# Kernel optimization log

Hardware: AMD Instinct MI355X
Metric: run time of the kernel (lower is better)

Reference implementation:

```python
import jax, jax.numpy as jnp
import numpy as np
import math

V, E, N, L, S_BLOCK, R = 50257, 1024, 16, 8, 1024, 4
B, S = 2, 1024
H = E // N
IPAD = 0


def layer_norm(x, w, b, eps=1e-5):
    mu = jnp.mean(x, axis=-1, keepdims=True)
    var = jnp.mean(jnp.square(x - mu), axis=-1, keepdims=True)
    return (x - mu) * jax.lax.rsqrt(var + eps) * w + b


def setup_inputs():
    key = jax.random.key(0)
    ks = jax.random.split(key, 10)
    nrm = lambda k, shape: jax.random.normal(k, shape, jnp.float32) * 0.02
    return {
        "x": jax.random.randint(ks[0], (B, S), 1, V, dtype=jnp.int32),
        "tok_emb": nrm(ks[1], (V, E)),
        "pos_emb": nrm(ks[2], (S_BLOCK, E)),
        "dec_ln_w": jnp.ones((E,), jnp.float32),
        "dec_ln_b": jnp.zeros((E,), jnp.float32),
        "qkv_w": nrm(ks[3], (L, 3 * E, E)),
        "qkv_b": jnp.zeros((L, 3 * E), jnp.float32),
        "attn_proj_w": nrm(ks[4], (L, E, E)),
        "attn_proj_b": jnp.zeros((L, E), jnp.float32),
        "ln1_w": jnp.ones((L, E), jnp.float32),
        "ln1_b": jnp.zeros((L, E), jnp.float32),
        "fc_w": nrm(ks[5], (L, R * E, E)),
        "fc_b": jnp.zeros((L, R * E), jnp.float32),
        "mlp_proj_w": nrm(ks[6], (L, E, R * E)),
        "mlp_proj_b": jnp.zeros((L, E), jnp.float32),
        "ln2_w": jnp.ones((L, E), jnp.float32),
        "ln2_b": jnp.zeros((L, E), jnp.float32),
        "fin_ln_w": jnp.ones((E,), jnp.float32),
        "fin_ln_b": jnp.zeros((E,), jnp.float32),
    }


def _forward(x, tok_emb, pos_emb, dec_ln_w, dec_ln_b, qkv_w, qkv_b,
             attn_proj_w, attn_proj_b, ln1_w, ln1_b, fc_w, fc_b,
             mlp_proj_w, mlp_proj_b, ln2_w, ln2_b, fin_ln_w, fin_ln_b):
    # token + positional embedding
    h = tok_emb[x] + pos_emb[:S][None, :, :]  # [B,S,E]
    # attention mask: causal AND key-not-pad (ipad=0, no cache -> C=0)
    causal = jnp.tril(jnp.ones((S, S), bool))  # [S,S]
    keypad = (x != IPAD)  # [B,S]
    mask = causal[None, None, :, :] & keypad[:, None, None, :]  # [B,1,S,S]
    scale = 1.0 / math.sqrt(H)

    # Decoder: ln then dropout(eval no-op) before blocks
    h = layer_norm(h, dec_ln_w, dec_ln_b)

    def block(h, p):
        (qw, qb, pw, pb, l1w, l1b, fw, fb, mw, mb, l2w, l2b) = p
        qkv = h @ qw.T + qb  # [B,S,3E]
        q, k, v = jnp.split(qkv, 3, axis=-1)
        q = q.reshape(B, S, N, H).transpose(0, 2, 1, 3)  # [B,N,S,H]
        k = k.reshape(B, S, N, H).transpose(0, 2, 1, 3)
        v = v.reshape(B, S, N, H).transpose(0, 2, 1, 3)
        scores = jnp.einsum('bnsh,bnth->bnst', q, k) * scale  # [B,N,S,S]
        scores = jnp.where(mask, scores, -jnp.inf)
        attn = jax.nn.softmax(scores, axis=-1)
        o = jnp.einsum('bnst,bnth->bnsh', attn, v)
        o = o.transpose(0, 2, 1, 3).reshape(B, S, E)
        o = o @ pw.T + pb
        h = layer_norm(o + h, l1w, l1b)  # post-norm
        m = jax.nn.gelu(h @ fw.T + fb, approximate=False) @ mw.T + mb
        h = layer_norm(m + h, l2w, l2b)
        return h, None

    params = (qkv_w, qkv_b, attn_proj_w, attn_proj_b, ln1_w, ln1_b,
              fc_w, fc_b, mlp_proj_w, mlp_proj_b, ln2_w, ln2_b)
    h, _ = jax.lax.scan(block, h, params)
    # final Transformer LayerNorm
    return layer_norm(h, fin_ln_w, fin_ln_b)


def reference(x, tok_emb, pos_emb, dec_ln_w, dec_ln_b, qkv_w, qkv_b,
              attn_proj_w, attn_proj_b, ln1_w, ln1_b, fc_w, fc_b,
              mlp_proj_w, mlp_proj_b, ln2_w, ln2_b, fin_ln_w, fin_ln_b):
    return _forward(x, tok_emb, pos_emb, dec_ln_w, dec_ln_b, qkv_w, qkv_b,
                    attn_proj_w, attn_proj_b, ln1_w, ln1_b, fc_w, fc_b,
                    mlp_proj_w, mlp_proj_b, ln2_w, ln2_b, fin_ln_w, fin_ln_b)
```

## Files before the change

### kernel.cpp

```cpp
#include <hip/hip_runtime.h>
#include <hip/hip_bf16.h>

#define E 1024
#define SLEN 1024
#define QKV3 3072
#define HD 64

typedef unsigned short u16;
typedef unsigned int   u32;
typedef __bf16 bf16x8 __attribute__((ext_vector_type(8)));
typedef float  f32x4  __attribute__((ext_vector_type(4)));
typedef float  fv4    __attribute__((ext_vector_type(4)));
typedef u32    uv2    __attribute__((ext_vector_type(2)));

__device__ __forceinline__ u16 f2bf(float f) {
  __hip_bfloat16 h = __float2bfloat16(f);
  return __builtin_bit_cast(u16, h);
}
__device__ __forceinline__ u32 pk2(float a, float b) {
  return (u32)f2bf(a) | ((u32)f2bf(b) << 16);
}
__device__ __forceinline__ uint4 pack8(const float4& x, const float4& y) {
  return make_uint4(pk2(x.x,x.y), pk2(x.z,x.w), pk2(y.x,y.y), pk2(y.z,y.w));
}

__device__ __forceinline__ void gload16(const u16* g, u16* l) {
  __builtin_amdgcn_global_load_lds(
      (const __attribute__((address_space(1))) void*)g,
      (__attribute__((address_space(3))) void*)l, 16, 0, 0);
}

__device__ __forceinline__ int swzP(int row, int ch) { return (row<<4) + (ch ^ (row & 7)); }

__global__ __launch_bounds__(256)
void f2b(const float* __restrict__ src, u16* __restrict__ dst, int n4)
{
  const int stride = gridDim.x * 256;
  const fv4* s4 = (const fv4*)src;
  uv2* d2 = (uv2*)dst;
  for (int i = blockIdx.x * 256 + threadIdx.x; i < n4; i += stride) {
    const fv4 v = __builtin_nontemporal_load(s4 + i);
    uv2 o; o.x = pk2(v.x, v.y); o.y = pk2(v.z, v.w);
    d2[i] = o;
  }
}

template<int BN, int OUTBF, int GELU, int SK>
__global__ __launch_bounds__(256)
void gemm_lds(const u16* __restrict__ A, const u16* __restrict__ W,
              const float* __restrict__ bias, void* __restrict__ Cv,
              int M, int N, int K)
{
  static_assert(!(GELU && SK > 1), "gelu needs full sum");
  static_assert(!(OUTBF && SK > 1), "partials are f32");
  constexpr int BM = 128;
  __shared__ __align__(16) u16 sA[3][BM*32];
  __shared__ __align__(16) u16 sB[3][BN*32];

  const int t = threadIdx.x;
  const int lane = t & 63;
  const int w = t >> 6;
  const int r = lane & 15;
  const int g = lane >> 4;
  const int wr = (w >> 1) * 64;
  const int wc = (w & 1) * (BN/2);

  const int row0 = blockIdx.y * BM;
  const int col0 = blockIdx.x * BN;
  const int k0   = (SK > 1) ? (int)blockIdx.z * (K / SK) : 0;

  constexpr int ACH = BM/16;
  constexpr int NCH = ACH + BN/16;
  constexpr int CPW = NCH/4;

  const int lrow = lane >> 2;
  const int lcol = (lane & 3) << 3;

  f32x4 acc[4][BN/32];
  #pragma unroll
  for (int i=0;i<4;i++)
    #pragma unroll
    for (int j=0;j<BN/32;j++)
      acc[i][j] = f32x4{0.f,0.f,0.f,0.f};

  const int nk = (K / SK) >> 5;

  auto stage = [&](int kt, int buf) {
    #pragma unroll
    for (int i = 0; i < CPW; ++i) {
      const int c = w*CPW + i;
      if (c < ACH) {
        const u16* gp = A + (size_t)(row0 + c*16 + lrow) * K + k0 + (kt<<5) + lcol;
        gload16(gp, &sA[buf][c*512]);
      } else {
        const int cb = c - ACH;
        const u16* gp = W + (size_t)(col0 + cb*16 + lrow) * K + k0 + (kt<<5) + lcol;
        gload16(gp, &sB[buf][cb*512]);
      }
    }
  };

  stage(0, 0);
  if (nk > 1) stage(1, 1);

  int cur = 0;
  for (int kt = 0; kt < nk; ++kt) {
    if (kt + 1 < nk) asm volatile("s_waitcnt vmcnt(4)" ::: "memory");
    else             asm volatile("s_waitcnt vmcnt(0)" ::: "memory");
    __builtin_amdgcn_s_barrier();

    if (kt + 2 < nk) stage(kt + 2, (cur + 2 >= 3) ? cur - 1 : cur + 2);

    bf16x8 af[4], bfr[BN/32];
    #pragma unroll
    for (int m=0;m<4;m++)
      af[m] = *(const bf16x8*)&sA[cur][(wr + (m<<4) + r)*32 + (g<<3)];
    #pragma unroll
    for (int n=0;n<BN/32;n++)
      bfr[n] = *(const bf16x8*)&sB[cur][(wc + (n<<4) + r)*32 + (g<<3)];
    #pragma unroll
    for (int m=0;m<4;m++)
      #pragma unroll
      for (int n=0;n<BN/32;n++)
        acc[m][n] = __builtin_amdgcn_mfma_f32_16x16x32_bf16(af[m], bfr[n], acc[m][n], 0, 0, 0);

    cur = (cur + 1 >= 3) ? 0 : cur + 1;
  }

  float* C32 = (float*)Cv + ((SK > 1) ? (size_t)blockIdx.z * M * N : 0);

  #pragma unroll
  for (int n=0;n<BN/32;n++) {
    const int col = col0 + wc + (n<<4) + r;
    const float bv = (SK == 1 || blockIdx.z == 0) ? bias[col] : 0.f;
    #pragma unroll
    for (int m=0;m<4;m++) {
      const int rowb = row0 + wr + (m<<4) + (g<<2);
      #pragma unroll
      for (int q=0;q<4;q++) {
        float v = acc[m][n][q] + bv;
        if (GELU) v = 0.5f * v * (1.f + erff(v * 0.70710678118f));
        if (OUTBF) ((u16*)Cv)[(size_t)(rowb + q) * N + col] = f2bf(v);
        else       C32[(size_t)(rowb + q) * N + col] = v;
      }
    }
  }
}

__global__ __launch_bounds__(256)
void attn_fwd(const u16* __restrict__ qkv, u16* __restrict__ o,
              float* __restrict__ opart, float* __restrict__ mpart,
              float* __restrict__ lpart)
{
  __shared__ __align__(16) u16 sK[128*64];
  __shared__ __align__(16) u16 sV[64*136];
  __shared__ __align__(16) u16 sP[4*32*128];

  const int j  = blockIdx.x;
  int qt, z, ns;
  if      (j < 3)  { qt = 7; z = j;      ns = 3; }
  else if (j < 6)  { qt = 6; z = j - 3;  ns = 3; }
  else if (j < 8)  { qt = 5; z = j - 6;  ns = 2; }
  else if (j < 10) { qt = 4; z = j - 8;  ns = 2; }
  else if (j < 12) { qt = 3; z = j - 10; ns = 2; }
  else             { qt = 14 - j; z = 0; ns = 1; }
  const int T = qt + 1, base = T / ns, rem = T % ns;
  const int kt0 = z * base + (z < rem ? z : rem);
  const int kt1 = kt0 + base + (z < rem ? 1 : 0);

  const int bn = blockIdx.y;
  const int b  = bn >> 4;
  const int hd = bn & 15;

  const int t = threadIdx.x;
  const int lane = t & 63;
  const int w = t >> 6;
  const int r = lane & 15;
  const int g = lane >> 4;

  const float SC = 0.125f * 1.44269504089f;

  bf16x8 qf[2][2];
  #pragma unroll
  for (int m=0;m<2;m++)
    #pragma unroll
    for (int kk=0;kk<2;kk++)
      qf[m][kk] = *(const bf16x8*)(qkv + (size_t)(b*SLEN + qt*128 + w*32 + (m<<4) + r) * QKV3
                                   + hd*HD + (kk<<5) + (g<<3));

  float m_run[2][4], l_run[2][4];
  f32x4 aco[2][4];
  #pragma unroll
  for (int m=0;m<2;m++) {
    #pragma unroll
    for (int q=0;q<4;q++) { m_run[m][q] = -1e30f; l_run[m][q] = 0.f; }
    #pragma unroll
    for (int n=0;n<4;n++) aco[m][n] = f32x4{0.f,0.f,0.f,0.f};
  }

  u16* sPw = sP + (w << 12);

  for (int kt = kt0; kt < kt1; ++kt) {
    __syncthreads();
    {
      const int rl = lane >> 3;
      const int hc = (lane & 7) ^ rl;
      #pragma unroll
      for (int i=0;i<4;i++) {
        const int c = w*4 + i;
        const u16* gp = qkv + (size_t)(b*SLEN + kt*128 + c*8 + rl) * QKV3
                      + E + hd*HD + (hc<<3);
        gload16(gp, &sK[c*512]);
      }
    }
    {
      const int vh = t & 63;
      const int tb = (t >> 6) << 5;
      const u16* vp = qkv + (size_t)(b*SLEN + kt*128 + tb) * QKV3 + 2*E + hd*HD + vh;
      #pragma unroll
      for (int i=0;i<32;i+=2) {
        const u32 v0 = vp[(size_t)i * QKV3];
        const u32 v1 = vp[(size_t)(i+1) * QKV3];
        const int tt = tb + i;
        const int gran = vh*17 + (tt >> 3);
        *(u32*)&sV[(gran<<3) + (tt & 7)] = v0 | (v1 << 16);
      }
    }
    __syncthreads();

    f32x4 s[2][8];
    #pragma unroll
    for (int m=0;m<2;m++)
      #pragma unroll
      for (int n=0;n<8;n++)
        s[m][n] = f32x4{0.f,0.f,0.f,0.f};
    __builtin_amdgcn_s_setprio(1);
    #pragma unroll
    for (int kk=0;kk<2;kk++) {
      bf16x8 kf[8];
      #pragma unroll
      for (int n=0;n<8;n++)
        kf[n] = *(const bf16x8*)&sK[((n<<4)+r)*64 + ((((kk<<2)+g) ^ (r&7))<<3)];
      #pragma unroll
      for (int m=0;m<2;m++)
        #pragma unroll
        for (int n=0;n<8;n++)
          s[m][n] = __builtin_amdgcn_mfma_f32_16x16x32_bf16(qf[m][kk], kf[n], s[m][n], 0,0,0);
    }
    __builtin_amdgcn_s_setprio(0);
    #pragma unroll
    for (int m=0;m<2;m++)
      #pragma unroll
      for (int n=0;n<8;n++)
        #pragma unroll
        for (int q=0;q<4;q++)
          s[m][n][q] *= SC;

    if (kt == qt) {
      #pragma unroll
      for (int m=0;m<2;m++)
        #pragma unroll
        for (int n=0;n<8;n++) {
          const int tg = (n<<4) + r;
          #pragma unroll
          for (int q=0;q<4;q++) {
            const int qg = w*32 + (m<<4) + (g<<2) + q;
            if (tg > qg) s[m][n][q] = -1e30f;
          }
        }
    }

    #pragma unroll
    for (int m=0;m<2;m++) {
      float f[4], rs[4];
      #pragma unroll
      for (int q=0;q<4;q++) {
        float v = s[m][0][q];
        #pragma unroll
        for (int n=1;n<8;n++) v = fmaxf(v, s[m][n][q]);
        v = fmaxf(v, __shfl_xor(v, 1));
        v = fmaxf(v, __shfl_xor(v, 2));
        v = fmaxf(v, __shfl_xor(v, 4));
        v = fmaxf(v, __shfl_xor(v, 8));
        const float mn = fmaxf(m_run[m][q], v);
        f[q] = exp2f(m_run[m][q] - mn);
        m_run[m][q] = mn;
        rs[q] = 0.f;
      }
      #pragma unroll
      for (int n=0;n<8;n++) {
        #pragma unroll
        for (int q=0;q<4;q++) {
          const float p = exp2f(s[m][n][q] - m_run[m][q]);
          rs[q] += p;
          const int prow = (m<<4) + (g<<2) + q;
          const int pch = (n<<1) + (r>>3);
          sPw[(swzP(prow, pch)<<3) + (r&7)] = f2bf(p);
        }
      }
      #pragma unroll
      for (int q=0;q<4;q++) {
        rs[q] += __shfl_xor(rs[q], 1);
        rs[q] += __shfl_xor(rs[q], 2);
        rs[q] += __shfl_xor(rs[q], 4);
        rs[q] += __shfl_xor(rs[q], 8);
        l_run[m][q] = l_run[m][q]*f[q] + rs[q];
      }
      #pragma unroll
      for (int n=0;n<4;n++)
        #pragma unroll
        for (int q=0;q<4;q++)
          aco[m][n][q] *= f[q];
    }

    __builtin_amdgcn_s_waitcnt(0);
    __builtin_amdgcn_sched_barrier(0);

    __builtin_amdgcn_s_setprio(1);
    #pragma unroll
    for (int kk=0;kk<4;kk++) {
      bf16x8 pf[2], vf[4];
      #pragma unroll
      for (int m=0;m<2;m++)
        pf[m] = *(const bf16x8*)&sPw[swzP((m<<4)+r, (kk<<2)+g)<<3];
      #pragma unroll
      for (int n=0;n<4;n++)
        vf[n] = *(const bf16x8*)&sV[(((n<<4)+r)*17 + (kk<<2) + g)<<3];
      #pragma unroll
      for (int m=0;m<2;m++)
        #pragma unroll
        for (int n=0;n<4;n++)
          aco[m][n] = __builtin_amdgcn_mfma_f32_16x16x32_bf16(pf[m], vf[n], aco[m][n], 0,0,0);
    }
    __builtin_amdgcn_s_setprio(0);
  }

  if (ns == 1) {
    #pragma unroll
    for (int m=0;m<2;m++)
      #pragma unroll
      for (int n=0;n<4;n++) {
        const int col = hd*HD + (n<<4) + r;
        #pragma unroll
        for (int q=0;q<4;q++) {
          const int qg = qt*128 + w*32 + (m<<4) + (g<<2) + q;
          o[(size_t)(b*SLEN + qg) * E + col] = f2bf(aco[m][n][q] / l_run[m][q]);
        }
      }
  } else {
    const size_t pb = (((size_t)z*32 + bn)*5 + (qt - 3)) * 128;
    float* op = opart + pb * 64;
    #pragma unroll
    for (int m=0;m<2;m++)
      #pragma unroll
      for (int n=0;n<4;n++) {
        #pragma unroll
        for (int q=0;q<4;q++) {
          const int row = w*32 + (m<<4) + (g<<2) + q;
          op[(size_t)row * 64 + (n<<4) + r] = aco[m][n][q];
        }
      }
    if (r == 0) {
      #pragma unroll
      for (int m=0;m<2;m++)
        #pragma unroll
        for (int q=0;q<4;q++) {
          const int row = w*32 + (m<<4) + (g<<2) + q;
          mpart[pb + row] = m_run[m][q];
          lpart[pb + row] = l_run[m][q];
        }
    }
  }
}

__global__ __launch_bounds__(256)
void attn_combine(const float* __restrict__ opart, const float* __restrict__ mpart,
                  const float* __restrict__ lpart, u16* __restrict__ o)
{
  const int qi = blockIdx.x;
  const int qt = qi + 3;
  const int np = (qt >= 6) ? 3 : 2;
  const int bn = blockIdx.y;
  const int b  = bn >> 4;
  const int hd = bn & 15;
  const int t = threadIdx.x;
  const int row = t >> 1;
  const int c0  = (t & 1) << 5;

  float4 acc[8];
  #pragma unroll
  for (int i=0;i<8;i++) acc[i] = make_float4(0.f,0.f,0.f,0.f);
  float m = -1e30f, l = 0.f;

  for (int z = 0; z < np; ++z) {
    const size_t pz = (((size_t)z*32 + bn)*5 + qi) * 128 + row;
    const float mz = mpart[pz], lz = lpart[pz];
    const float nm = fmaxf(m, mz);
    const float fo = exp2f(m - nm), fn = exp2f(mz - nm);
    const float4* oz = (const float4*)(opart + pz*64 + c0);
    #pragma unroll
    for (int i=0;i<8;i++) {
      const float4 v = oz[i];
      acc[i].x = acc[i].x*fo + v.x*fn;
      acc[i].y = acc[i].y*fo + v.y*fn;
      acc[i].z = acc[i].z*fo + v.z*fn;
      acc[i].w = acc[i].w*fo + v.w*fn;
    }
    l = l*fo + lz*fn;
    m = nm;
  }
  const float inv = 1.f / l;
  u16* ob = o + (size_t)(b*SLEN + qt*128 + row) * E + hd*HD + c0;
  #pragma unroll
  for (int i=0;i<8;i++) {
    uint2 pk; pk.x = pk2(acc[i].x*inv, acc[i].y*inv); pk.y = pk2(acc[i].z*inv, acc[i].w*inv);
    ((uint2*)ob)[i] = pk;
  }
}

__global__ __launch_bounds__(256)
void ln_row(const float* __restrict__ a, const float* __restrict__ a2,
            const float* __restrict__ res,
            const float* __restrict__ lw, const float* __restrict__ lb,
            float* __restrict__ out32, u16* __restrict__ outb)
{
  __shared__ float red[8];
  const int row = blockIdx.x;
  const int i = threadIdx.x;
  float4 v = ((const float4*)(a + ((size_t)row << 10)))[i];
  if (a2 != nullptr) {
    const float4 rv = ((const float4*)(a2 + ((size_t)row << 10)))[i];
    v.x += rv.x; v.y += rv.y; v.z += rv.z; v.w += rv.w;
  }
  if (res != nullptr) {
    const float4 rv = ((const float4*)(res + ((size_t)row << 10)))[i];
    v.x += rv.x; v.y += rv.y; v.z += rv.z; v.w += rv.w;
  }
  float s1 = v.x + v.y + v.z + v.w;
  float s2 = v.x*v.x + v.y*v.y + v.z*v.z + v.w*v.w;
  #pragma unroll
  for (int off=1; off<64; off<<=1) { s1 += __shfl_xor(s1, off); s2 += __shfl_xor(s2, off); }
  if ((i & 63) == 0) { red[(i>>6)*2] = s1; red[(i>>6)*2+1] = s2; }
  __syncthreads();
  s1 = red[0] + red[2] + red[4] + red[6];
  s2 = red[1] + red[3] + red[5] + red[7];
  const float mean = s1 * (1.f/1024.f);
  const float var  = s2 * (1.f/1024.f) - mean*mean;
  const float rstd = rsqrtf(var + 1e-5f);
  const float4 wv = ((const float4*)lw)[i];
  const float4 bv = ((const float4*)lb)[i];
  float4 ov;
  ov.x = (v.x - mean)*rstd*wv.x + bv.x;
  ov.y = (v.y - mean)*rstd*wv.y + bv.y;
  ov.z = (v.z - mean)*rstd*wv.z + bv.z;
  ov.w = (v.w - mean)*rstd*wv.w + bv.w;
  if (out32) ((float4*)(out32 + ((size_t)row << 10)))[i] = ov;
  if (outb) {
    uint2 pk; pk.x = pk2(ov.x, ov.y); pk.y = pk2(ov.z, ov.w);
    ((uint2*)(outb + ((size_t)row << 10)))[i] = pk;
  }
}

__global__ __launch_bounds__(256)
void embed_ln(const int* __restrict__ x, const float* __restrict__ tok,
              const float* __restrict__ pos, const float* __restrict__ lw,
              const float* __restrict__ lb, float* __restrict__ h32,
              u16* __restrict__ hb)
{
  __shared__ float red[8];
  const int row = blockIdx.x;
  const int s = row & (SLEN-1);
  const int i = threadIdx.x;
  const int id = x[row];
  const float4 tv = ((const float4*)(tok + ((size_t)id << 10)))[i];
  const float4 pv = ((const float4*)(pos + ((size_t)s << 10)))[i];
  float4 v;
  v.x = tv.x + pv.x; v.y = tv.y + pv.y; v.z = tv.z + pv.z; v.w = tv.w + pv.w;
  float s1 = v.x + v.y + v.z + v.w;
  float s2 = v.x*v.x + v.y*v.y + v.z*v.z + v.w*v.w;
  #pragma unroll
  for (int off=1; off<64; off<<=1) { s1 += __shfl_xor(s1, off); s2 += __shfl_xor(s2, off); }
  if ((i & 63) == 0) { red[(i>>6)*2] = s1; red[(i>>6)*2+1] = s2; }
  __syncthreads();
  s1 = red[0] + red[2] + red[4] + red[6];
  s2 = red[1] + red[3] + red[5] + red[7];
  const float mean = s1 * (1.f/1024.f);
  const float var  = s2 * (1.f/1024.f) - mean*mean;
  const float rstd = rsqrtf(var + 1e-5f);
  const float4 wv = ((const float4*)lw)[i];
  const float4 bv = ((const float4*)lb)[i];
  float4 ov;
  ov.x = (v.x - mean)*rstd*wv.x + bv.x;
  ov.y = (v.y - mean)*rstd*wv.y + bv.y;
  ov.z = (v.z - mean)*rstd*wv.z + bv.z;
  ov.w = (v.w - mean)*rstd*wv.w + bv.w;
  ((float4*)(h32 + ((size_t)row << 10)))[i] = ov;
  uint2 pk; pk.x = pk2(ov.x, ov.y); pk.y = pk2(ov.z, ov.w);
  ((uint2*)(hb + ((size_t)row << 10)))[i] = pk;
}

extern "C" void kernel_launch(void* const* d_in, const int* in_sizes, int n_in,
                              void* d_out, int out_size, void* d_ws, size_t ws_size,
                              hipStream_t stream) {
  const int*   x    = (const int*)  d_in[0];
  const float* tok  = (const float*)d_in[1];
  const float* pos  = (const float*)d_in[2];
  const float* decw = (const float*)d_in[3];
  const float* decb = (const float*)d_in[4];
  const float* qkvw = (const float*)d_in[5];
  const float* qkvb = (const float*)d_in[6];
  const float* apw  = (const float*)d_in[7];
  const float* apb  = (const float*)d_in[8];
  const float* l1w  = (const float*)d_in[9];
  const float* l1b  = (const float*)d_in[10];
  const float* fcw  = (const float*)d_in[11];
  const float* fcb  = (const float*)d_in[12];
  const float* mpw  = (const float*)d_in[13];
  const float* mpb  = (const float*)d_in[14];
  const float* l2w  = (const float*)d_in[15];
  const float* l2b  = (const float*)d_in[16];
  const float* finw = (const float*)d_in[17];
  const float* finb = (const float*)d_in[18];
  float* out = (float*)d_out;

  char* p = (char*)d_ws;
  float* h32   = (float*)p;                p += (size_t)2048*1024*4;
  float* part  = (float*)p;                p += (size_t)2*2048*1024*4;
  float* opart = (float*)p;                p += (size_t)3*32*5*128*64*4;
  float* mpart = (float*)p;                p += (size_t)3*32*5*128*4;
  float* lpart = (float*)p;                p += (size_t)3*32*5*128*4;
  u16*   hb    = (u16*)p;                  p += (size_t)2048*1024*2;
  u16*   qkvB  = (u16*)p;                  p += (size_t)2048*3072*2;
  u16*   ab    = (u16*)p;                  p += (size_t)2048*1024*2;
  u16*   fb    = (u16*)p;                  p += (size_t)2048*4096*2;
  u16*   wq    = (u16*)p;                  p += (size_t)8*3072*1024*2;
  u16*   wap   = (u16*)p;                  p += (size_t)8*1024*1024*2;
  u16*   wfc   = (u16*)p;                  p += (size_t)8*4096*1024*2;
  u16*   wmp   = (u16*)p;                  p += (size_t)8*4096*1024*2;
  float* part1 = part + (size_t)2048*1024;

  f2b<<<2048, 256, 0, stream>>>(qkvw, wq,  8*3072*1024/4);
  f2b<<<1024, 256, 0, stream>>>(apw,  wap, 8*1024*1024/4);
  f2b<<<2048, 256, 0, stream>>>(fcw,  wfc, 8*4096*1024/4);
  f2b<<<2048, 256, 0, stream>>>(mpw,  wmp, 8*4096*1024/4);

  embed_ln<<<2048, 256, 0, stream>>>(x, tok, pos, decw, decb, h32, hb);

  for (int l = 0; l < 8; ++l) {
    const u16* lwq  = wq  + (size_t)l*3072*1024;
    const u16* lwap = wap + (size_t)l*1024*1024;
    const u16* lwfc = wfc + (size_t)l*4096*1024;
    const u16* lwmp = wmp + (size_t)l*4096*1024;

    gemm_lds<128,1,0,1><<<dim3(24,16),   256, 0, stream>>>(hb, lwq,  qkvb + (size_t)l*3072, qkvB, 2048, 3072, 1024);
    attn_fwd<<<dim3(15,32), 256, 0, stream>>>(qkvB, ab, opart, mpart, lpart);
    attn_combine<<<dim3(5,32), 256, 0, stream>>>(opart, mpart, lpart, ab);
    gemm_lds<128,0,0,2><<<dim3(8,16,2),  256, 0, stream>>>(ab, lwap, apb + (size_t)l*1024, part, 2048, 1024, 1024);
    ln_row<<<2048, 256, 0, stream>>>(part, part1, h32, l1w + (size_t)l*1024, l1b + (size_t)l*1024, h32, hb);
    gemm_lds<128,1,1,1><<<dim3(32,16),   256, 0, stream>>>(hb, lwfc, fcb + (size_t)l*4096, fb, 2048, 4096, 1024);
    gemm_lds<128,0,0,2><<<dim3(8,16,2),  256, 0, stream>>>(fb, lwmp, mpb + (size_t)l*1024, part, 2048, 1024, 4096);
    ln_row<<<2048, 256, 0, stream>>>(part, part1, h32, l2w + (size_t)l*1024, l2b + (size_t)l*1024, h32, hb);
  }

  ln_row<<<2048, 256, 0, stream>>>(h32, nullptr, nullptr, finw, finb, out, nullptr);
}
```

Baseline: 1.414 ms.

## Store split-K partials and residual stream in bf16, add XCD-aware block swizzle

```diff
diff --git a/kernel.cpp b/kernel.cpp
--- a/kernel.cpp
+++ b/kernel.cpp
@@ -20,8 +20,9 @@
 __device__ __forceinline__ u32 pk2(float a, float b) {
   return (u32)f2bf(a) | ((u32)f2bf(b) << 16);
 }
-__device__ __forceinline__ uint4 pack8(const float4& x, const float4& y) {
-  return make_uint4(pk2(x.x,x.y), pk2(x.z,x.w), pk2(y.x,y.y), pk2(y.z,y.w));
+__device__ __forceinline__ float bf2f(u32 lo16) {
+  const u32 b = lo16 << 16;
+  return __builtin_bit_cast(float, b);
 }
 
 __device__ __forceinline__ void gload16(const u16* g, u16* l) {
@@ -45,17 +46,33 @@
   }
 }
 
-template<int BN, int OUTBF, int GELU, int SK>
+template<int BN, int OUTBF, int GELU, int SK, int SWCX, int SWCY>
 __global__ __launch_bounds__(256)
 void gemm_lds(const u16* __restrict__ A, const u16* __restrict__ W,
               const float* __restrict__ bias, void* __restrict__ Cv,
               int M, int N, int K)
 {
   static_assert(!(GELU && SK > 1), "gelu needs full sum");
-  static_assert(!(OUTBF && SK > 1), "partials are f32");
   constexpr int BM = 128;
   __shared__ __align__(16) u16 sA[3][BM*32];
   __shared__ __align__(16) u16 sB[3][BN*32];
+
+  int bx, by, bz;
+  if (SWCX > 0) {
+    const int gx = gridDim.x, gy = gridDim.y;
+    const int bid = blockIdx.x + gx*(blockIdx.y + gy*blockIdx.z);
+    const int nchx = gx / SWCX;
+    const int nchy = gy / SWCY;
+    const int xcd = bid & 7;
+    const int within = bid >> 3;
+    const int cz  = xcd / (nchx*nchy);
+    const int rem = xcd % (nchx*nchy);
+    bx = (rem % nchx)*SWCX + within % SWCX;
+    by = (rem / nchx)*SWCY + within / SWCX;
+    bz = cz;
+  } else {
+    bx = blockIdx.x; by = blockIdx.y; bz = blockIdx.z;
+  }
 
   const int t = threadIdx.x;
   const int lane = t & 63;
@@ -65,9 +82,9 @@
   const int wr = (w >> 1) * 64;
   const int wc = (w & 1) * (BN/2);
 
-  const int row0 = blockIdx.y * BM;
-  const int col0 = blockIdx.x * BN;
-  const int k0   = (SK > 1) ? (int)blockIdx.z * (K / SK) : 0;
+  const int row0 = by * BM;
+  const int col0 = bx * BN;
+  const int k0   = (SK > 1) ? bz * (K / SK) : 0;
 
   constexpr int ACH = BM/16;
   constexpr int NCH = ACH + BN/16;
@@ -127,12 +144,13 @@
     cur = (cur + 1 >= 3) ? 0 : cur + 1;
   }
 
-  float* C32 = (float*)Cv + ((SK > 1) ? (size_t)blockIdx.z * M * N : 0);
+  u16*   Cb  = (u16*)Cv   + ((SK > 1) ? (size_t)bz * M * N : 0);
+  float* C32 = (float*)Cv;
 
   #pragma unroll
   for (int n=0;n<BN/32;n++) {
     const int col = col0 + wc + (n<<4) + r;
-    const float bv = (SK == 1 || blockIdx.z == 0) ? bias[col] : 0.f;
+    const float bv = (SK == 1 || bz == 0) ? bias[col] : 0.f;
     #pragma unroll
     for (int m=0;m<4;m++) {
       const int rowb = row0 + wr + (m<<4) + (g<<2);
@@ -140,7 +158,7 @@
       for (int q=0;q<4;q++) {
         float v = acc[m][n][q] + bv;
         if (GELU) v = 0.5f * v * (1.f + erff(v * 0.70710678118f));
-        if (OUTBF) ((u16*)Cv)[(size_t)(rowb + q) * N + col] = f2bf(v);
+        if (OUTBF) Cb[(size_t)(rowb + q) * N + col] = f2bf(v);
         else       C32[(size_t)(rowb + q) * N + col] = v;
       }
     }
@@ -419,23 +437,31 @@
 }
 
 __global__ __launch_bounds__(256)
-void ln_row(const float* __restrict__ a, const float* __restrict__ a2,
-            const float* __restrict__ res,
-            const float* __restrict__ lw, const float* __restrict__ lb,
-            float* __restrict__ out32, u16* __restrict__ outb)
+void ln_bf(const u16* __restrict__ a0, const u16* __restrict__ a1,
+           const u16* __restrict__ res,
+           const float* __restrict__ lw, const float* __restrict__ lb,
+           u16* __restrict__ outb, float* __restrict__ out32)
 {
   __shared__ float red[8];
   const int row = blockIdx.x;
   const int i = threadIdx.x;
-  float4 v = ((const float4*)(a + ((size_t)row << 10)))[i];
-  if (a2 != nullptr) {
-    const float4 rv = ((const float4*)(a2 + ((size_t)row << 10)))[i];
-    v.x += rv.x; v.y += rv.y; v.z += rv.z; v.w += rv.w;
+  const size_t base = (size_t)row << 10;
+
+  uint2 pk0 = ((const uint2*)(a0 + base))[i];
+  float4 v;
+  v.x = bf2f(pk0.x & 0xffff); v.y = bf2f(pk0.x >> 16);
+  v.z = bf2f(pk0.y & 0xffff); v.w = bf2f(pk0.y >> 16);
+  if (a1 != nullptr) {
+    uint2 pk1 = ((const uint2*)(a1 + base))[i];
+    v.x += bf2f(pk1.x & 0xffff); v.y += bf2f(pk1.x >> 16);
+    v.z += bf2f(pk1.y & 0xffff); v.w += bf2f(pk1.y >> 16);
   }
   if (res != nullptr) {
-    const float4 rv = ((const float4*)(res + ((size_t)row << 10)))[i];
-    v.x += rv.x; v.y += rv.y; v.z += rv.z; v.w += rv.w;
-  }
+    uint2 pk1 = ((const uint2*)(res + base))[i];
+    v.x += bf2f(pk1.x & 0xffff); v.y += bf2f(pk1.x >> 16);
+    v.z += bf2f(pk1.y & 0xffff); v.w += bf2f(pk1.y >> 16);
+  }
+
   float s1 = v.x + v.y + v.z + v.w;
   float s2 = v.x*v.x + v.y*v.y + v.z*v.z + v.w*v.w;
   #pragma unroll
@@ -454,18 +480,17 @@
   ov.y = (v.y - mean)*rstd*wv.y + bv.y;
   ov.z = (v.z - mean)*rstd*wv.z + bv.z;
   ov.w = (v.w - mean)*rstd*wv.w + bv.w;
-  if (out32) ((float4*)(out32 + ((size_t)row << 10)))[i] = ov;
   if (outb) {
     uint2 pk; pk.x = pk2(ov.x, ov.y); pk.y = pk2(ov.z, ov.w);
-    ((uint2*)(outb + ((size_t)row << 10)))[i] = pk;
-  }
+    ((uint2*)(outb + base))[i] = pk;
+  }
+  if (out32) ((float4*)(out32 + base))[i] = ov;
 }
 
 __global__ __launch_bounds__(256)
 void embed_ln(const int* __restrict__ x, const float* __restrict__ tok,
               const float* __restrict__ pos, const float* __restrict__ lw,
-              const float* __restrict__ lb, float* __restrict__ h32,
-              u16* __restrict__ hb)
+              const float* __restrict__ lb, u16* __restrict__ hb)
 {
   __shared__ float red[8];
   const int row = blockIdx.x;
@@ -494,7 +519,6 @@
   ov.y = (v.y - mean)*rstd*wv.y + bv.y;
   ov.z = (v.z - mean)*rstd*wv.z + bv.z;
   ov.w = (v.w - mean)*rstd*wv.w + bv.w;
-  ((float4*)(h32 + ((size_t)row << 10)))[i] = ov;
   uint2 pk; pk.x = pk2(ov.x, ov.y); pk.y = pk2(ov.z, ov.w);
   ((uint2*)(hb + ((size_t)row << 10)))[i] = pk;
 }
@@ -524,11 +548,10 @@
   float* out = (float*)d_out;
 
   char* p = (char*)d_ws;
-  float* h32   = (float*)p;                p += (size_t)2048*1024*4;
-  float* part  = (float*)p;                p += (size_t)2*2048*1024*4;
   float* opart = (float*)p;                p += (size_t)3*32*5*128*64*4;
   float* mpart = (float*)p;                p += (size_t)3*32*5*128*4;
   float* lpart = (float*)p;                p += (size_t)3*32*5*128*4;
+  u16*   partb = (u16*)p;                  p += (size_t)2*2048*1024*2;
   u16*   hb    = (u16*)p;                  p += (size_t)2048*1024*2;
   u16*   qkvB  = (u16*)p;                  p += (size_t)2048*3072*2;
   u16*   ab    = (u16*)p;                  p += (size_t)2048*1024*2;
@@ -537,14 +560,14 @@
   u16*   wap   = (u16*)p;                  p += (size_t)8*1024*1024*2;
   u16*   wfc   = (u16*)p;                  p += (size_t)8*4096*1024*2;
   u16*   wmp   = (u16*)p;                  p += (size_t)8*4096*1024*2;
-  float* part1 = part + (size_t)2048*1024;
+  u16*   partb1 = partb + (size_t)2048*1024;
 
   f2b<<<2048, 256, 0, stream>>>(qkvw, wq,  8*3072*1024/4);
   f2b<<<1024, 256, 0, stream>>>(apw,  wap, 8*1024*1024/4);
   f2b<<<2048, 256, 0, stream>>>(fcw,  wfc, 8*4096*1024/4);
   f2b<<<2048, 256, 0, stream>>>(mpw,  wmp, 8*4096*1024/4);
 
-  embed_ln<<<2048, 256, 0, stream>>>(x, tok, pos, decw, decb, h32, hb);
+  embed_ln<<<2048, 256, 0, stream>>>(x, tok, pos, decw, decb, hb);
 
   for (int l = 0; l < 8; ++l) {
     const u16* lwq  = wq  + (size_t)l*3072*1024;
@@ -552,15 +575,15 @@
     const u16* lwfc = wfc + (size_t)l*4096*1024;
     const u16* lwmp = wmp + (size_t)l*4096*1024;
 
-    gemm_lds<128,1,0,1><<<dim3(24,16),   256, 0, stream>>>(hb, lwq,  qkvb + (size_t)l*3072, qkvB, 2048, 3072, 1024);
+    gemm_lds<128,1,0,1,6,8><<<dim3(24,16),  256, 0, stream>>>(hb, lwq,  qkvb + (size_t)l*3072, qkvB, 2048, 3072, 1024);
     attn_fwd<<<dim3(15,32), 256, 0, stream>>>(qkvB, ab, opart, mpart, lpart);
     attn_combine<<<dim3(5,32), 256, 0, stream>>>(opart, mpart, lpart, ab);
-    gemm_lds<128,0,0,2><<<dim3(8,16,2),  256, 0, stream>>>(ab, lwap, apb + (size_t)l*1024, part, 2048, 1024, 1024);
-    ln_row<<<2048, 256, 0, stream>>>(part, part1, h32, l1w + (size_t)l*1024, l1b + (size_t)l*1024, h32, hb);
-    gemm_lds<128,1,1,1><<<dim3(32,16),   256, 0, stream>>>(hb, lwfc, fcb + (size_t)l*4096, fb, 2048, 4096, 1024);
-    gemm_lds<128,0,0,2><<<dim3(8,16,2),  256, 0, stream>>>(fb, lwmp, mpb + (size_t)l*1024, part, 2048, 1024, 4096);
-    ln_row<<<2048, 256, 0, stream>>>(part, part1, h32, l2w + (size_t)l*1024, l2b + (size_t)l*1024, h32, hb);
-  }
-
-  ln_row<<<2048, 256, 0, stream>>>(h32, nullptr, nullptr, finw, finb, out, nullptr);
-}
+    gemm_lds<128,1,0,2,4,8><<<dim3(8,16,2), 256, 0, stream>>>(ab, lwap, apb + (size_t)l*1024, partb, 2048, 1024, 1024);
+    ln_bf<<<2048, 256, 0, stream>>>(partb, partb1, hb, l1w + (size_t)l*1024, l1b + (size_t)l*1024, hb, nullptr);
+    gemm_lds<128,1,1,1,8,8><<<dim3(32,16),  256, 0, stream>>>(hb, lwfc, fcb + (size_t)l*4096, fb, 2048, 4096, 1024);
+    gemm_lds<128,1,0,2,4,8><<<dim3(8,16,2), 256, 0, stream>>>(fb, lwmp, mpb + (size_t)l*1024, partb, 2048, 1024, 4096);
+    ln_bf<<<2048, 256, 0, stream>>>(partb, partb1, hb, l2w + (size_t)l*1024, l2b + (size_t)l*1024, hb, nullptr);
+  }
+
+  ln_bf<<<2048, 256, 0, stream>>>(hb, nullptr, nullptr, finw, finb, nullptr, out);
+}
```

Measured after the change: 1.318 ms. -6.8%, faster.
